# Optimization experiments

Hardware: AMD Instinct MI355X
Metric: run time of the kernel (lower is better)

The kernel has to match this reference:

```python
import jax, jax.numpy as jnp
import numpy as np

B, H, S, D = 4, 16, 2048, 128


def setup_inputs() -> dict:
    key0 = jax.random.key(0)
    kq, kk, kv, km = jax.random.split(key0, 4)
    query = jax.random.normal(kq, (B, H, S, D), dtype=jnp.float32)
    key = jax.random.normal(kk, (B, H, S, D), dtype=jnp.float32)
    value = jax.random.normal(kv, (B, H, S, D), dtype=jnp.float32)
    mask = jax.random.normal(km, (1, 1, S, S), dtype=jnp.float32)
    return {"query": query, "key": key, "value": value, "mask": mask}


def reference(query, key, value, mask):
    # qk: [B, H, S, S]
    qk = jnp.einsum('bhqd,bhkd->bhqk', query, key)
    qk = qk + mask
    # NOTE: original module divides by sqrt(D) AFTER adding the mask
    scale = 1.0 / jnp.sqrt(jnp.asarray(key.shape[-1], dtype=query.dtype))
    attn = jax.nn.softmax(qk * scale, axis=-1)
    return jnp.einsum('bhqk,bhkd->bhqd', attn, value)
```

## Files before the change

### kernel.cpp

```cpp
#include <hip/hip_runtime.h>
#include <math.h>

#define SEQ   2048
#define HD    128
#define KVB   64
#define NT    (SEQ / KVB)
#define SCALE_L2E 0.12753242193263556f

typedef __bf16 bf16_t;
typedef __bf16 bf16x2 __attribute__((ext_vector_type(2)));
typedef __bf16 bf16x4 __attribute__((ext_vector_type(4)));
typedef __bf16 bf16x8 __attribute__((ext_vector_type(8)));
typedef float  f32x16 __attribute__((ext_vector_type(16)));

__device__ __forceinline__ void gl_lds16(const void* g, void* l) {
  __builtin_amdgcn_global_load_lds(
      (const __attribute__((address_space(1))) unsigned int*)g,
      (__attribute__((address_space(3))) unsigned int*)l, 16, 0, 0);
}

__global__ __launch_bounds__(256)
void mk_kimg(const float* __restrict__ k, char* __restrict__ img) {
  const int bt = blockIdx.x;
  const float* src = k + (size_t)bt * KVB * HD;
  char* dst = img + (size_t)bt * 16384;
  const int tid = threadIdx.x;
#pragma unroll
  for (int i = 0; i < 8; ++i) {
    const int g = tid + i * 256;
    const int r = g >> 5, c4 = g & 31;
    float4 v = *(const float4*)(src + (size_t)r * HD + c4 * 4);
    const int o = (r * 256 + c4 * 8) ^ ((r & 7) << 4);
    *(bf16x4*)(dst + o) = bf16x4{(bf16_t)v.x, (bf16_t)v.y, (bf16_t)v.z, (bf16_t)v.w};
  }
}

__global__ __launch_bounds__(256)
void mk_vimg(const float* __restrict__ v, char* __restrict__ img) {
  __shared__ float tile[KVB][HD + 4];
  const int bt = blockIdx.x;
  const float* src = v + (size_t)bt * KVB * HD;
  char* dst = img + (size_t)bt * 16384;
  const int tid = threadIdx.x;
#pragma unroll
  for (int i = 0; i < 8; ++i) {
    const int g = tid + i * 256;
    const int r = g >> 5, c4 = g & 31;
    float4 a = *(const float4*)(src + (size_t)r * HD + c4 * 4);
    tile[r][c4 * 4 + 0] = a.x; tile[r][c4 * 4 + 1] = a.y;
    tile[r][c4 * 4 + 2] = a.z; tile[r][c4 * 4 + 3] = a.w;
  }
  __syncthreads();
#pragma unroll
  for (int i = 0; i < 8; ++i) {
    const int g = tid + i * 256;
    const int o = g * 8;
    const int d = o >> 7;
    const int inner = (o & 127) ^ ((d & 7) << 4);
    const int pe0 = inner >> 1;
    bf16x4 w;
#pragma unroll
    for (int e = 0; e < 4; ++e) {
      const int pe = pe0 + e;
      const int a  = pe >> 4;
      const int bp = pe & 15;
      const int vv = bp >> 1;
      const int sv = (vv & 1) | ((vv & 2) << 1) | ((vv & 4) >> 1);
      const int kk = a * 16 + sv * 2 + (bp & 1);
      w[e] = (bf16_t)tile[kk][d];
    }
    *(bf16x4*)(dst + o) = w;
  }
}

__global__ __launch_bounds__(256)
void mask_tr2(const float* __restrict__ m, bf16x2* __restrict__ mt2) {
  __shared__ float tile[32][65];
  const int tid = threadIdx.x;
  const int k0  = blockIdx.x * 64;
  const int q0  = blockIdx.y * 32;
#pragma unroll
  for (int i = 0; i < 2; ++i) {
    const int ix = tid + i * 256;
    const int qr = ix >> 4, c4 = ix & 15;
    float4 v = *(const float4*)(m + (size_t)(q0 + qr) * SEQ + k0 + c4 * 4);
    tile[qr][c4 * 4 + 0] = v.x; tile[qr][c4 * 4 + 1] = v.y;
    tile[qr][c4 * 4 + 2] = v.z; tile[qr][c4 * 4 + 3] = v.w;
  }
  __syncthreads();
#pragma unroll
  for (int i = 0; i < 4; ++i) {
    const int ix = tid + i * 256;
    const int kl = ix >> 5, qq = ix & 31;
    mt2[(size_t)(blockIdx.x * 32 + kl) * SEQ + q0 + qq] =
        bf16x2{(bf16_t)(tile[qq][kl] * SCALE_L2E),
               (bf16_t)(tile[qq][kl + 32] * SCALE_L2E)};
  }
}

__global__ __launch_bounds__(256)
void mask_tr(const float* __restrict__ m, float* __restrict__ mt) {
  __shared__ float tile[32][33];
  const int tx = threadIdx.x & 31;
  const int ty = threadIdx.x >> 5;
  const int kb = blockIdx.x * 32;
  const int qb = blockIdx.y * 32;
#pragma unroll
  for (int r = 0; r < 32; r += 8)
    tile[ty + r][tx] = m[(size_t)(qb + ty + r) * SEQ + kb + tx] * SCALE_L2E;
  __syncthreads();
#pragma unroll
  for (int r = 0; r < 32; r += 8)
    mt[(size_t)(kb + ty + r) * SEQ + qb + tx] = tile[tx][ty + r];
}

__global__ __launch_bounds__(256, 2)
void attn_fwd_v3(const float* __restrict__ q_g, const char* __restrict__ kimg,
                 const char* __restrict__ vimg, const bf16x2* __restrict__ mt2_g,
                 float* __restrict__ o_g) {
  __shared__ __align__(16) char ldsK[2][KVB * 256];
  __shared__ __align__(16) char ldsV[2][HD * 128];

  const int tid  = threadIdx.x;
  const int wid  = tid >> 6;
  const int lane = tid & 63;
  const int hi   = lane >> 5;
  const int ql   = lane & 31;

  const int lin = blockIdx.x;
  const int xcd = lin & 7;
  const int idx = lin >> 3;
  const int bh  = xcd + 8 * (idx >> 4);
  const int q0  = (idx & 15) * 128;

  const float* Qb = q_g + (size_t)bh * SEQ * HD;
  float*       Ob = o_g + (size_t)bh * SEQ * HD;

  const int qrow = q0 + wid * 32 + ql;

  bf16x8 qf[8];
#pragma unroll
  for (int kd = 0; kd < 8; ++kd) {
    const float* p = Qb + (size_t)qrow * HD + kd * 16 + hi * 8;
    float4 a = *(const float4*)p;
    float4 b = *(const float4*)(p + 4);
    qf[kd] = bf16x8{(bf16_t)a.x, (bf16_t)a.y, (bf16_t)a.z, (bf16_t)a.w,
                    (bf16_t)b.x, (bf16_t)b.y, (bf16_t)b.z, (bf16_t)b.w};
  }

  f32x16 ot[4];
#pragma unroll
  for (int dt = 0; dt < 4; ++dt)
#pragma unroll
    for (int r = 0; r < 16; ++r) ot[dt][r] = 0.f;

  float m_run = -INFINITY, l_run = 0.f;

#define STAGE(T, BUF)                                                        \
  { const char* gK = kimg + ((size_t)bh * NT + (T)) * 16384 + wid * 4096 +   \
                     lane * 16;                                              \
    const char* gV = vimg + ((size_t)bh * NT + (T)) * 16384 + wid * 4096 +   \
                     lane * 16;                                              \
    char* lK = ldsK[BUF] + wid * 4096;                                       \
    char* lV = ldsV[BUF] + wid * 4096;                                       \
    _Pragma("unroll") for (int j = 0; j < 4; ++j) {                          \
      gl_lds16(gK + j * 1024, lK + j * 1024);                                \
      gl_lds16(gV + j * 1024, lV + j * 1024);                                \
    } }

  STAGE(0, 0)

  for (int t = 0; t < NT; ++t) {
    __syncthreads();
    const int buf = t & 1;
    const char* Kl = ldsK[buf];
    const char* Vl = ldsV[buf];
    const bool more = (t + 1 < NT);

    bf16x2 mreg[16];
    {
      const bf16x2* MTp = mt2_g + (size_t)(t * 32) * SEQ + qrow;
#pragma unroll
      for (int r = 0; r < 16; ++r) {
        const int kl = (r & 3) + 8 * (r >> 2) + 4 * hi;
        mreg[r] = MTp[(size_t)kl * SEQ];
      }
    }

    if (more) { STAGE(t + 1, buf ^ 1) }

    f32x16 s0, s1;
#pragma unroll
    for (int r = 0; r < 16; ++r) { s0[r] = 0.f; s1[r] = 0.f; }
#pragma unroll
    for (int kd = 0; kd < 8; ++kd) {
      int b0 = ql * 256 + kd * 32 + hi * 16; b0 ^= (ql & 7) << 4;
      bf16x8 kf0 = *(const bf16x8*)(Kl + b0);
      bf16x8 kf1 = *(const bf16x8*)(Kl + b0 + 8192);
      s0 = __builtin_amdgcn_mfma_f32_32x32x16_bf16(kf0, qf[kd], s0, 0, 0, 0);
      s1 = __builtin_amdgcn_mfma_f32_32x32x16_bf16(kf1, qf[kd], s1, 0, 0, 0);
    }

    float x0[16], x1[16];
#pragma unroll
    for (int r = 0; r < 16; ++r) {
      x0[r] = fmaf(s0[r], SCALE_L2E, (float)mreg[r][0]);
      x1[r] = fmaf(s1[r], SCALE_L2E, (float)mreg[r][1]);
    }
    float tm[16];
#pragma unroll
    for (int r = 0; r < 16; ++r) tm[r] = fmaxf(x0[r], x1[r]);
#pragma unroll
    for (int off = 8; off > 0; off >>= 1)
#pragma unroll
      for (int r = 0; r < off; ++r) tm[r] = fmaxf(tm[r], tm[r + off]);
    const float mx   = fmaxf(tm[0], __shfl_xor(tm[0], 32, 64));
    const float mnew = fmaxf(m_run, mx);
    const float fac  = __builtin_amdgcn_exp2f(m_run - mnew);
    m_run = mnew;

    float p0[16], p1[16];
#pragma unroll
    for (int r = 0; r < 16; ++r) {
      p0[r] = __builtin_amdgcn_exp2f(x0[r] - mnew);
      p1[r] = __builtin_amdgcn_exp2f(x1[r] - mnew);
    }
    float ts[16];
#pragma unroll
    for (int r = 0; r < 16; ++r) ts[r] = p0[r] + p1[r];
#pragma unroll
    for (int off = 8; off > 0; off >>= 1)
#pragma unroll
      for (int r = 0; r < off; ++r) ts[r] += ts[r + off];
    const float sum = ts[0] + __shfl_xor(ts[0], 32, 64);
    l_run = l_run * fac + sum;

#pragma unroll
    for (int dt = 0; dt < 4; ++dt)
#pragma unroll
      for (int r = 0; r < 16; ++r) ot[dt][r] *= fac;

    bf16x8 pb[2][2];
#pragma unroll
    for (int kf = 0; kf < 2; ++kf) {
      pb[0][kf] = bf16x8{(bf16_t)p0[8*kf+0], (bf16_t)p0[8*kf+1],
                         (bf16_t)p0[8*kf+2], (bf16_t)p0[8*kf+3],
                         (bf16_t)p0[8*kf+4], (bf16_t)p0[8*kf+5],
                         (bf16_t)p0[8*kf+6], (bf16_t)p0[8*kf+7]};
      pb[1][kf] = bf16x8{(bf16_t)p1[8*kf+0], (bf16_t)p1[8*kf+1],
                         (bf16_t)p1[8*kf+2], (bf16_t)p1[8*kf+3],
                         (bf16_t)p1[8*kf+4], (bf16_t)p1[8*kf+5],
                         (bf16_t)p1[8*kf+6], (bf16_t)p1[8*kf+7]};
    }

#pragma unroll
    for (int tt = 0; tt < 2; ++tt)
#pragma unroll
      for (int kf = 0; kf < 2; ++kf) {
        const int kg = tt * 2 + kf;
#pragma unroll
        for (int dt = 0; dt < 4; ++dt) {
          const int d = dt * 32 + ql;
          int byt = d * 128 + kg * 32 + hi * 16; byt ^= (d & 7) << 4;
          bf16x8 vf = *(const bf16x8*)(Vl + byt);
          ot[dt] = __builtin_amdgcn_mfma_f32_32x32x16_bf16(vf, pb[tt][kf], ot[dt], 0, 0, 0);
        }
      }
  }

  const float rinv = 1.f / l_run;
  float* Op = Ob + (size_t)qrow * HD;
#pragma unroll
  for (int dt = 0; dt < 4; ++dt)
#pragma unroll
    for (int r = 0; r < 16; ++r) {
      const int d = dt * 32 + (r & 3) + 8 * (r >> 2) + 4 * hi;
      Op[d] = ot[dt][r] * rinv;
    }
}

__global__ __launch_bounds__(256, 2)
void attn_fwd_fb(const float* __restrict__ q_g, const float* __restrict__ k_g,
                 const float* __restrict__ v_g, const float* __restrict__ mt_g,
                 float* __restrict__ o_g) {
  __shared__ __align__(16) char ldsK[2][KVB * 256];
  __shared__ __align__(16) char ldsV[2][HD * 128];

  const int tid  = threadIdx.x;
  const int wid  = tid >> 6;
  const int lane = tid & 63;
  const int hi   = lane >> 5;
  const int ql   = lane & 31;

  const int lin = blockIdx.x;
  const int xcd = lin & 7;
  const int idx = lin >> 3;
  const int bh  = xcd + 8 * (idx >> 4);
  const int q0  = (idx & 15) * 128;

  const float* Qb = q_g + (size_t)bh * SEQ * HD;
  const float* Kb = k_g + (size_t)bh * SEQ * HD;
  const float* Vb = v_g + (size_t)bh * SEQ * HD;
  float*       Ob = o_g + (size_t)bh * SEQ * HD;

  const int qrow = q0 + wid * 32 + ql;

  bf16x8 qf[8];
#pragma unroll
  for (int kd = 0; kd < 8; ++kd) {
    const float* p = Qb + (size_t)qrow * HD + kd * 16 + hi * 8;
    float4 a = *(const float4*)p;
    float4 b = *(const float4*)(p + 4);
    qf[kd] = bf16x8{(bf16_t)a.x, (bf16_t)a.y, (bf16_t)a.z, (bf16_t)a.w,
                    (bf16_t)b.x, (bf16_t)b.y, (bf16_t)b.z, (bf16_t)b.w};
  }

  f32x16 ot[4];
#pragma unroll
  for (int dt = 0; dt < 4; ++dt)
#pragma unroll
    for (int r = 0; r < 16; ++r) ot[dt][r] = 0.f;

  float m_run = -INFINITY, l_run = 0.f;

  float4 kreg[8], vA[4], vB[4];
  const int vp  = tid & 31;
  const int vcb = tid >> 5;
  const int vkb = ((vp >> 3) << 5) +
                  (((vp & 1) | ((vp & 2) << 1) | ((vp & 4) >> 1)) << 2);

#define KF_ISSUE(K0)                                                         \
  { _Pragma("unroll") for (int i = 0; i < 8; ++i) {                          \
      const int ix = tid + i * 256;                                          \
      kreg[i] = *(const float4*)(Kb + (size_t)((K0) + (ix >> 5)) * HD +      \
                                 (ix & 31) * 4); } }

#define KF_WRITE(BUF)                                                        \
  { char* dK = ldsK[BUF];                                                    \
    _Pragma("unroll") for (int i = 0; i < 8; ++i) {                          \
      const int ix = tid + i * 256;                                          \
      const int row = ix >> 5; const int c4 = ix & 31;                       \
      int byt = row * 256 + c4 * 8; byt ^= (row & 7) << 4;                   \
      float4 v = kreg[i];                                                    \
      *(bf16x4*)(dK + byt) =                                                 \
          bf16x4{(bf16_t)v.x, (bf16_t)v.y, (bf16_t)v.z, (bf16_t)v.w}; } }

#define VF_ISSUE_A(K0)                                                       \
  { _Pragma("unroll") for (int i = 0; i < 2; ++i) {                          \
      const int c4 = vcb + 8 * i;                                            \
      vA[2*i]   = *(const float4*)(Vb + (size_t)((K0) + 2*vp)     * HD + c4*4); \
      vA[2*i+1] = *(const float4*)(Vb + (size_t)((K0) + 2*vp + 1) * HD + c4*4); } }

#define VF_ISSUE_B(K0)                                                       \
  { _Pragma("unroll") for (int i = 0; i < 2; ++i) {                          \
      const int c4 = vcb + 16 + 8 * i;                                       \
      vB[2*i]   = *(const float4*)(Vb + (size_t)((K0) + 2*vp)     * HD + c4*4); \
      vB[2*i+1] = *(const float4*)(Vb + (size_t)((K0) + 2*vp + 1) * HD + c4*4); } }

#define VF_WRITE_X(BUF, REGS, COFF)                                          \
  { char* dV = ldsV[BUF];                                                    \
    _Pragma("unroll") for (int i = 0; i < 2; ++i) {                          \
      const int c4 = vcb + (COFF) + 8 * i;                                   \
      const float* r0 = (const float*)&REGS[2*i];                            \
      const float* r1 = (const float*)&REGS[2*i+1];                          \
      _Pragma("unroll") for (int j = 0; j < 4; ++j) {                        \
        const int d = c4 * 4 + j;                                            \
        int byt = d * 128 + vkb; byt ^= (d & 7) << 4;                        \
        *(bf16x2*)(dV + byt) = bf16x2{(bf16_t)r0[j], (bf16_t)r1[j]}; } } }

  KF_ISSUE(0)
  VF_ISSUE_A(0)
  VF_ISSUE_B(0)
  KF_WRITE(0)
  VF_WRITE_X(0, vA, 0)
  VF_WRITE_X(0, vB, 16)

  for (int t = 0; t < NT; ++t) {
    __syncthreads();
    const int buf = t & 1;
    const char* Kl = ldsK[buf];
    const char* Vl = ldsV[buf];
    const bool more = (t + 1 < NT);

    if (more) { KF_ISSUE((t + 1) * KVB) }

    float mk0[16], mk1[16];
    {
      const float* MTp = mt_g + (size_t)(t * KVB) * SEQ + qrow;
#pragma unroll
      for (int r = 0; r < 16; ++r) {
        const int k = (r & 3) + 8 * (r >> 2) + 4 * hi;
        mk0[r] = MTp[(size_t)k * SEQ];
        mk1[r] = MTp[(size_t)(k + 32) * SEQ];
      }
    }

    if (more) { VF_ISSUE_A((t + 1) * KVB) }

    f32x16 s0, s1;
#pragma unroll
    for (int r = 0; r < 16; ++r) { s0[r] = 0.f; s1[r] = 0.f; }
#pragma unroll
    for (int kd = 0; kd < 8; ++kd) {
      int b0 = ql * 256 + kd * 32 + hi * 16; b0 ^= (ql & 7) << 4;
      bf16x8 kf0 = *(const bf16x8*)(Kl + b0);
      bf16x8 kf1 = *(const bf16x8*)(Kl + b0 + 8192);
      s0 = __builtin_amdgcn_mfma_f32_32x32x16_bf16(kf0, qf[kd], s0, 0, 0, 0);
      s1 = __builtin_amdgcn_mfma_f32_32x32x16_bf16(kf1, qf[kd], s1, 0, 0, 0);
    }

    if (more) {
      VF_WRITE_X(buf ^ 1, vA, 0)
      VF_ISSUE_B((t + 1) * KVB)
    }

    float x0[16], x1[16];
#pragma unroll
    for (int r = 0; r < 16; ++r) {
      x0[r] = fmaf(s0[r], SCALE_L2E, mk0[r]);
      x1[r] = fmaf(s1[r], SCALE_L2E, mk1[r]);
    }
    float tm[16];
#pragma unroll
    for (int r = 0; r < 16; ++r) tm[r] = fmaxf(x0[r], x1[r]);
#pragma unroll
    for (int off = 8; off > 0; off >>= 1)
#pragma unroll
      for (int r = 0; r < off; ++r) tm[r] = fmaxf(tm[r], tm[r + off]);
    const float mx   = fmaxf(tm[0], __shfl_xor(tm[0], 32, 64));
    const float mnew = fmaxf(m_run, mx);
    const float fac  = __builtin_amdgcn_exp2f(m_run - mnew);
    m_run = mnew;

    float p0[16], p1[16];
#pragma unroll
    for (int r = 0; r < 16; ++r) {
      p0[r] = __builtin_amdgcn_exp2f(x0[r] - mnew);
      p1[r] = __builtin_amdgcn_exp2f(x1[r] - mnew);
    }
    float ts[16];
#pragma unroll
    for (int r = 0; r < 16; ++r) ts[r] = p0[r] + p1[r];
#pragma unroll
    for (int off = 8; off > 0; off >>= 1)
#pragma unroll
      for (int r = 0; r < off; ++r) ts[r] += ts[r + off];
    const float sum = ts[0] + __shfl_xor(ts[0], 32, 64);
    l_run = l_run * fac + sum;

#pragma unroll
    for (int dt = 0; dt < 4; ++dt)
#pragma unroll
      for (int r = 0; r < 16; ++r) ot[dt][r] *= fac;

    bf16x8 pb[2][2];
#pragma unroll
    for (int kf = 0; kf < 2; ++kf) {
      pb[0][kf] = bf16x8{(bf16_t)p0[8*kf+0], (bf16_t)p0[8*kf+1],
                         (bf16_t)p0[8*kf+2], (bf16_t)p0[8*kf+3],
                         (bf16_t)p0[8*kf+4], (bf16_t)p0[8*kf+5],
                         (bf16_t)p0[8*kf+6], (bf16_t)p0[8*kf+7]};
      pb[1][kf] = bf16x8{(bf16_t)p1[8*kf+0], (bf16_t)p1[8*kf+1],
                         (bf16_t)p1[8*kf+2], (bf16_t)p1[8*kf+3],
                         (bf16_t)p1[8*kf+4], (bf16_t)p1[8*kf+5],
                         (bf16_t)p1[8*kf+6], (bf16_t)p1[8*kf+7]};
    }

#pragma unroll
    for (int tt = 0; tt < 2; ++tt)
#pragma unroll
      for (int kf = 0; kf < 2; ++kf) {
        const int kg = tt * 2 + kf;
#pragma unroll
        for (int dt = 0; dt < 4; ++dt) {
          const int d = dt * 32 + ql;
          int byt = d * 128 + kg * 32 + hi * 16; byt ^= (d & 7) << 4;
          bf16x8 vf = *(const bf16x8*)(Vl + byt);
          ot[dt] = __builtin_amdgcn_mfma_f32_32x32x16_bf16(vf, pb[tt][kf], ot[dt], 0, 0, 0);
        }
      }

    if (more) {
      VF_WRITE_X(buf ^ 1, vB, 16)
      KF_WRITE(buf ^ 1)
    }
  }

  const float rinv = 1.f / l_run;
  float* Op = Ob + (size_t)qrow * HD;
#pragma unroll
  for (int dt = 0; dt < 4; ++dt)
#pragma unroll
    for (int r = 0; r < 16; ++r) {
      const int d = dt * 32 + (r & 3) + 8 * (r >> 2) + 4 * hi;
      Op[d] = ot[dt][r] * rinv;
    }
}

extern "C" void kernel_launch(void* const* d_in, const int* in_sizes, int n_in,
                              void* d_out, int out_size, void* d_ws, size_t ws_size,
                              hipStream_t stream) {
  (void)in_sizes; (void)n_in; (void)out_size;
  const float* Q = (const float*)d_in[0];
  const float* K = (const float*)d_in[1];
  const float* V = (const float*)d_in[2];
  const float* M = (const float*)d_in[3];
  float*       O = (float*)d_out;

  const size_t szImg = (size_t)64 * NT * 16384;
  const size_t szM2  = (size_t)(SEQ / KVB) * 32 * SEQ * 4;

  if (ws_size >= 2 * szImg + szM2) {
    char*   KI  = (char*)d_ws;
    char*   VI  = (char*)d_ws + szImg;
    bf16x2* MT2 = (bf16x2*)((char*)d_ws + 2 * szImg);
    mk_kimg<<<64 * NT, 256, 0, stream>>>(K, KI);
    mk_vimg<<<64 * NT, 256, 0, stream>>>(V, VI);
    mask_tr2<<<dim3(SEQ / 64, SEQ / 32), 256, 0, stream>>>(M, MT2);
    attn_fwd_v3<<<dim3(1024), 256, 0, stream>>>(Q, KI, VI, MT2, O);
  } else {
    float* MT = (float*)d_ws;
    mask_tr<<<dim3(SEQ / 32, SEQ / 32), 256, 0, stream>>>(M, MT);
    attn_fwd_fb<<<dim3(1024), 256, 0, stream>>>(Q, K, V, MT, O);
  }
}
```

Baseline: 235.8 us.

## Single-buffer K in LDS and prefetch next K tile after QK MFMAs

K is now single-buffered in LDS instead of double-buffered. The next K tile is issued right after the QK^T MFMAs, behind an extra barrier, so its load overlaps the softmax and PV work. V stays double-buffered. This cuts LDS per block from 64KB to 48KB, which could let more blocks fit per CU, at the cost of one more __syncthreads per iteration and a shorter prefetch window for K.

```diff
diff --git a/kernel.cpp b/kernel.cpp
--- a/kernel.cpp
+++ b/kernel.cpp
@@ -115,10 +115,10 @@
 }
 
 __global__ __launch_bounds__(256, 2)
-void attn_fwd_v3(const float* __restrict__ q_g, const char* __restrict__ kimg,
+void attn_fwd_v5(const float* __restrict__ q_g, const char* __restrict__ kimg,
                  const char* __restrict__ vimg, const bf16x2* __restrict__ mt2_g,
                  float* __restrict__ o_g) {
-  __shared__ __align__(16) char ldsK[2][KVB * 256];
+  __shared__ __align__(16) char ldsK[KVB * 256];
   __shared__ __align__(16) char ldsV[2][HD * 128];
 
   const int tid  = threadIdx.x;
@@ -156,25 +156,27 @@
 
   float m_run = -INFINITY, l_run = 0.f;
 
-#define STAGE(T, BUF)                                                        \
+#define STAGE_K(T)                                                           \
   { const char* gK = kimg + ((size_t)bh * NT + (T)) * 16384 + wid * 4096 +   \
                      lane * 16;                                              \
-    const char* gV = vimg + ((size_t)bh * NT + (T)) * 16384 + wid * 4096 +   \
+    char* lK = ldsK + wid * 4096;                                            \
+    _Pragma("unroll") for (int j = 0; j < 4; ++j)                            \
+      gl_lds16(gK + j * 1024, lK + j * 1024); }
+
+#define STAGE_V(T, BUF)                                                      \
+  { const char* gV = vimg + ((size_t)bh * NT + (T)) * 16384 + wid * 4096 +   \
                      lane * 16;                                              \
-    char* lK = ldsK[BUF] + wid * 4096;                                       \
     char* lV = ldsV[BUF] + wid * 4096;                                       \
-    _Pragma("unroll") for (int j = 0; j < 4; ++j) {                          \
-      gl_lds16(gK + j * 1024, lK + j * 1024);                                \
-      gl_lds16(gV + j * 1024, lV + j * 1024);                                \
-    } }
-
-  STAGE(0, 0)
+    _Pragma("unroll") for (int j = 0; j < 4; ++j)                            \
+      gl_lds16(gV + j * 1024, lV + j * 1024); }
+
+  STAGE_K(0)
+  STAGE_V(0, 0)
 
   for (int t = 0; t < NT; ++t) {
     __syncthreads();
-    const int buf = t & 1;
-    const char* Kl = ldsK[buf];
-    const char* Vl = ldsV[buf];
+    const int vbuf = t & 1;
+    const char* Vl = ldsV[vbuf];
     const bool more = (t + 1 < NT);
 
     bf16x2 mreg[16];
@@ -187,7 +189,7 @@
       }
     }
 
-    if (more) { STAGE(t + 1, buf ^ 1) }
+    if (more) { STAGE_V(t + 1, vbuf ^ 1) }
 
     f32x16 s0, s1;
 #pragma unroll
@@ -195,11 +197,15 @@
 #pragma unroll
     for (int kd = 0; kd < 8; ++kd) {
       int b0 = ql * 256 + kd * 32 + hi * 16; b0 ^= (ql & 7) << 4;
-      bf16x8 kf0 = *(const bf16x8*)(Kl + b0);
-      bf16x8 kf1 = *(const bf16x8*)(Kl + b0 + 8192);
+      bf16x8 kf0 = *(const bf16x8*)(ldsK + b0);
+      bf16x8 kf1 = *(const bf16x8*)(ldsK + b0 + 8192);
       s0 = __builtin_amdgcn_mfma_f32_32x32x16_bf16(kf0, qf[kd], s0, 0, 0, 0);
       s1 = __builtin_amdgcn_mfma_f32_32x32x16_bf16(kf1, qf[kd], s1, 0, 0, 0);
     }
+
+    __syncthreads();
+
+    if (more) { STAGE_K(t + 1) }
 
     float x0[16], x1[16];
 #pragma unroll
@@ -517,7 +523,7 @@
     mk_kimg<<<64 * NT, 256, 0, stream>>>(K, KI);
     mk_vimg<<<64 * NT, 256, 0, stream>>>(V, VI);
     mask_tr2<<<dim3(SEQ / 64, SEQ / 32), 256, 0, stream>>>(M, MT2);
-    attn_fwd_v3<<<dim3(1024), 256, 0, stream>>>(Q, KI, VI, MT2, O);
+    attn_fwd_v5<<<dim3(1024), 256, 0, stream>>>(Q, KI, VI, MT2, O);
   } else {
     float* MT = (float*)d_ws;
     mask_tr<<<dim3(SEQ / 32, SEQ / 32), 256, 0, stream>>>(M, MT);
```

New measurement: 235.8 us. About the same (+0.0%).
